# Performance work log

Hardware: AMD Instinct MI355X
Metric: run time of the kernel (lower is better)

## Reference

```python
import jax, jax.numpy as jnp
import numpy as np

B, L, D, K = 16, 4096, 256, 64
RHO, LAMBDA_Q, LAMBDA_S = 0.5, 1.0, 1.0


def setup_inputs() -> dict:
    key = jax.random.key(0)
    ks = jax.random.split(key, 16)
    s = 1.0 / np.sqrt(D)
    inp = {
        'q': jax.random.normal(ks[0], (B, D), jnp.float32),
        'r_pos': jax.random.normal(ks[1], (B, D), jnp.float32),
        'r_neg': jax.random.normal(ks[2], (B, D), jnp.float32),
        'h': jax.random.normal(ks[3], (B, L, D), jnp.float32),
        'rp': jax.random.normal(ks[4], (B, L, D), jnp.float32),
        'rn': jax.random.normal(ks[5], (B, L, D), jnp.float32),
        'lengths': jnp.maximum(1, jax.random.randint(ks[6], (B,), 0, L, jnp.int32)),
        'proto_idx': 3,
        'prototypes': jax.random.normal(ks[7], (K, D), jnp.float32),
        'W_hist_w': jax.random.normal(ks[8], (D, 2 * D), jnp.float32) * s,
        'W_hist_b': jnp.zeros((D,), jnp.float32),
        'Wq_w': jax.random.normal(ks[9], (D, D), jnp.float32) * s,
        'Wq_b': jnp.zeros((D,), jnp.float32),
        'Ws_w': jax.random.normal(ks[10], (D, D), jnp.float32) * s,
        'Ws_b': jnp.zeros((D,), jnp.float32),
    }
    return inp


def reference(q, r_pos, r_neg, h, rp, rn, lengths, proto_idx, prototypes,
              W_hist_w, W_hist_b, Wq_w, Wq_b, Ws_w, Ws_b):
    d = q.shape[-1]
    scale = 1.0 / jnp.sqrt(jnp.asarray(d, q.dtype))
    a = prototypes[proto_idx]                                   # [d]
    # gather + tanh-MLP over padded events: inp = [h, rp-rn] -> [B,L,2d]
    inp = jnp.concatenate([h, rp - rn], axis=-1)
    o = jnp.tanh(jnp.einsum('ble,de->bld', inp, W_hist_w) + W_hist_b)  # [B,L,d]
    # attention logits against prototype and query
    logits = (jnp.einsum('bld,d->bl', o, a)
              + RHO * jnp.einsum('bld,bd->bl', o, q)) * scale   # [B,L]
    mask = jnp.arange(o.shape[1])[None, :] < lengths[:, None]   # [B,L]
    logits = jnp.where(mask, logits, -1e30)
    alpha = jax.nn.softmax(logits, axis=1)
    s_q = jnp.einsum('bl,bld->bd', alpha, o)                    # [B,d]
    z = (a[None, :]
         + LAMBDA_Q * (q @ Wq_w.T + Wq_b)
         + LAMBDA_S * (s_q @ Ws_w.T + Ws_b))                    # [B,d]
    delta = jnp.sum(z * (r_pos - r_neg), axis=-1)               # [B]
    # BCE-with-logits against all-ones targets: mean softplus(-delta)
    l_pair = jnp.mean(jax.nn.softplus(-delta))
    return l_pair
```

## Files before the change

### kernel.cpp

```cpp
#include <hip/hip_runtime.h>

#define B_      16
#define L_      4096
#define D_      256
#define K2_     512
#define TILE_M  64
#define BK      64
#define KITERS  8
#define PSTRIDE 264

typedef float f32x4 __attribute__((ext_vector_type(4)));
typedef short bf16x8 __attribute__((ext_vector_type(8)));

__device__ __forceinline__ unsigned short f2bf(float x) {
    unsigned int u = __float_as_uint(x);
    u += 0x7FFF + ((u >> 16) & 1);
    return (unsigned short)(u >> 16);
}
__device__ __forceinline__ unsigned int pk2(float a, float b) {
    return (unsigned int)f2bf(a) | ((unsigned int)f2bf(b) << 16);
}
__device__ __forceinline__ bf16x8 pack8(f32x4 a, f32x4 b) {
    union { bf16x8 v; unsigned int u[4]; } r;
    r.u[0] = pk2(a[0], a[1]); r.u[1] = pk2(a[2], a[3]);
    r.u[2] = pk2(b[0], b[1]); r.u[3] = pk2(b[2], b[3]);
    return r.v;
}
__device__ __forceinline__ void gload_lds16(const void* g, void* l) {
    __builtin_amdgcn_global_load_lds(
        (const __attribute__((address_space(1))) unsigned int*)g,
        (__attribute__((address_space(3))) unsigned int*)l, 16, 0, 0);
}
__device__ __forceinline__ float fast_tanh(float x) {
    float e = __expf(2.0f * x);
    return 1.0f - __fdividef(2.0f, e + 1.0f);
}

__global__ __launch_bounds__(256) void prep_kernel(
    const float* __restrict__ Wh, const float* __restrict__ protos,
    const float* __restrict__ q, const int* __restrict__ pidx,
    const int* __restrict__ lengths,
    unsigned short* __restrict__ wsW, float* __restrict__ aeff,
    int* __restrict__ tiles, int* __restrict__ tileCnt)
{
    const int blk = blockIdx.x, tid = threadIdx.x;
    if (blk < 256) {
        int d  = blk;
        int e  = tid * 2;
        int t  = e >> 6;
        int kk = e & 63;
        float2 w = *reinterpret_cast<const float2*>(Wh + d * K2_ + e);
        unsigned int v = pk2(w.x, w.y);
        int dst = t * 32768 + ((d * 128 + kk * 2) ^ ((d & 7) << 4));
        *reinterpret_cast<unsigned int*>(reinterpret_cast<char*>(wsW) + dst) = v;
    } else if (blk < 272) {
        int b = blk - 256;
        int d = tid;
        int pi = pidx[0];
        aeff[b * D_ + d] = (protos[pi * D_ + d] + 0.5f * q[b * D_ + d]) * 0.0625f;
    } else {
        int nT = 0;
        if (tid < B_) nT = min(64, (lengths[tid] + TILE_M - 1) / TILE_M);
        int pre = 0, tot = 0;
#pragma unroll
        for (int j = 0; j < B_; ++j) {
            int v = __shfl(nT, j, 64);
            tot += v;
            if (j < tid) pre += v;
        }
        if (tid < B_) {
            for (int t = 0; t < nT; ++t) tiles[pre + t] = (tid << 16) | t;
        }
        if (tid == 0) tileCnt[0] = tot;
    }
}

__global__ __launch_bounds__(256, 2) void main_kernel(
    const float* __restrict__ h, const float* __restrict__ rp, const float* __restrict__ rn,
    const int* __restrict__ lengths, const unsigned short* __restrict__ wsW,
    const float* __restrict__ aeff, const float* __restrict__ bhist,
    float* __restrict__ partials, const int* __restrict__ tiles,
    const int* __restrict__ tileCnt)
{
    const int bid = blockIdx.x;
    if (bid >= tileCnt[0]) return;
    const int ent = tiles[bid];
    const int b   = ent >> 16;
    const int t   = ent & 0xFFFF;
    const int len = lengths[b];
    const int l0  = t * TILE_M;

    __shared__ __align__(16) char Bsm[65536];
    __shared__ float red[128];
    __shared__ float pbuf[64];
    __shared__ float solds[4 * 128];

    const int tid  = threadIdx.x;
    const int lane = tid & 63;
    const int wv   = tid >> 6;
    const int rg   = wv >> 1;
    const int ch   = wv & 1;
    const int r16  = lane & 15;
    const int kg   = lane >> 4;

    const size_t rowA0 = ((size_t)b * L_ + l0 + rg * 32 + r16) * D_ + kg * 8;

    const f32x4 zero4 = {0.f, 0.f, 0.f, 0.f};
    f32x4 acc[2][8];
#pragma unroll
    for (int m = 0; m < 2; ++m)
#pragma unroll
        for (int n = 0; n < 8; ++n) acc[m][n] = zero4;

    f32x4 pA[2][2][2], pB[2][2][2];
    bf16x8 frag[2][2];

    auto stageB = [&](int buf, int tk) {
        const char* bsrc = reinterpret_cast<const char*>(wsW) + tk * 32768;
        char* dst = Bsm + buf * 32768;
#pragma unroll
        for (int i = 0; i < 8; ++i) {
            int off = i * 4096 + wv * 1024;
            gload_lds16(bsrc + off + lane * 16, dst + off);
        }
    };
    auto loadA = [&](int tk) {
        if (tk < 4) {
            const float* p0 = h + rowA0 + tk * 64;
#pragma unroll
            for (int m = 0; m < 2; ++m) {
                const float* p = p0 + m * 16 * D_;
#pragma unroll
                for (int ks = 0; ks < 2; ++ks) {
                    pA[m][ks][0] = *reinterpret_cast<const f32x4*>(p + ks * 32);
                    pA[m][ks][1] = *reinterpret_cast<const f32x4*>(p + ks * 32 + 4);
                }
            }
        } else {
            size_t o0 = rowA0 + (tk - 4) * 64;
#pragma unroll
            for (int m = 0; m < 2; ++m) {
                size_t o = o0 + (size_t)m * 16 * D_;
#pragma unroll
                for (int ks = 0; ks < 2; ++ks) {
                    pA[m][ks][0] = *reinterpret_cast<const f32x4*>(rp + o + ks * 32);
                    pA[m][ks][1] = *reinterpret_cast<const f32x4*>(rp + o + ks * 32 + 4);
                    pB[m][ks][0] = *reinterpret_cast<const f32x4*>(rn + o + ks * 32);
                    pB[m][ks][1] = *reinterpret_cast<const f32x4*>(rn + o + ks * 32 + 4);
                }
            }
        }
    };
    auto cvtA = [&](int tk) {
#pragma unroll
        for (int m = 0; m < 2; ++m)
#pragma unroll
            for (int ks = 0; ks < 2; ++ks) {
                f32x4 v0, v1;
                if (tk < 4) { v0 = pA[m][ks][0]; v1 = pA[m][ks][1]; }
                else        { v0 = pA[m][ks][0] - pB[m][ks][0]; v1 = pA[m][ks][1] - pB[m][ks][1]; }
                frag[m][ks] = pack8(v0, v1);
            }
    };
    auto computeT = [&](int buf) {
        const char* Bb = Bsm + buf * 32768;
#pragma unroll
        for (int ks = 0; ks < 2; ++ks) {
#pragma unroll
            for (int nt = 0; nt < 8; ++nt) {
                int d   = ch * 128 + nt * 16 + r16;
                int off = (d * 128 + (ks * 32 + kg * 8) * 2) ^ ((d & 7) << 4);
                bf16x8 bfr = *reinterpret_cast<const bf16x8*>(Bb + off);
                acc[0][nt] = __builtin_amdgcn_mfma_f32_16x16x32_bf16(frag[0][ks], bfr, acc[0][nt], 0, 0, 0);
                acc[1][nt] = __builtin_amdgcn_mfma_f32_16x16x32_bf16(frag[1][ks], bfr, acc[1][nt], 0, 0, 0);
            }
        }
    };

    loadA(0);
    stageB(0, 0);
    cvtA(0);
    __syncthreads();

    int buf = 0;
    for (int tk = 0; tk < KITERS; ++tk) {
        const bool pf = (tk + 1) < KITERS;
        if (pf) { loadA(tk + 1); stageB(buf ^ 1, tk + 1); }
        __builtin_amdgcn_sched_barrier(0);
        computeT(buf);
        if (pf) cvtA(tk + 1);
        __syncthreads();
        buf ^= 1;
    }

    float av[8], bh[8];
#pragma unroll
    for (int nt = 0; nt < 8; ++nt) {
        int col = ch * 128 + nt * 16 + r16;
        av[nt] = aeff[b * D_ + col];
        bh[nt] = bhist[col];
    }
    float part[2][4];
#pragma unroll
    for (int m = 0; m < 2; ++m)
#pragma unroll
        for (int rgi = 0; rgi < 4; ++rgi) part[m][rgi] = 0.f;
#pragma unroll
    for (int m = 0; m < 2; ++m)
#pragma unroll
        for (int nt = 0; nt < 8; ++nt)
#pragma unroll
            for (int rgi = 0; rgi < 4; ++rgi) {
                float o = fast_tanh(acc[m][nt][rgi] + bh[nt]);
                acc[m][nt][rgi] = o;
                part[m][rgi] += o * av[nt];
            }
#pragma unroll
    for (int off = 1; off < 16; off <<= 1)
#pragma unroll
        for (int m = 0; m < 2; ++m)
#pragma unroll
            for (int rgi = 0; rgi < 4; ++rgi)
                part[m][rgi] += __shfl_xor(part[m][rgi], off, 64);
    if (r16 == 0) {
#pragma unroll
        for (int m = 0; m < 2; ++m)
#pragma unroll
            for (int rgi = 0; rgi < 4; ++rgi)
                red[ch * 64 + rg * 32 + m * 16 + kg * 4 + rgi] = part[m][rgi];
    }
    __syncthreads();

    float* pout = partials + (size_t)(b * 64 + t) * PSTRIDE;
    if (tid < 64) {
        int row = tid;
        float lg = red[row] + red[64 + row];
        bool valid = (l0 + row) < len;
        float mv = valid ? lg : -3.0e38f;
#pragma unroll
        for (int off = 1; off < 64; off <<= 1)
            mv = fmaxf(mv, __shfl_xor(mv, off, 64));
        float p = valid ? __expf(lg - mv) : 0.f;
        float sa = p;
#pragma unroll
        for (int off = 1; off < 64; off <<= 1)
            sa += __shfl_xor(sa, off, 64);
        pbuf[row] = p;
        if (tid == 0) { pout[0] = mv; pout[1] = sa; }
    }
    __syncthreads();

    float so[8];
#pragma unroll
    for (int nt = 0; nt < 8; ++nt) so[nt] = 0.f;
#pragma unroll
    for (int m = 0; m < 2; ++m)
#pragma unroll
        for (int rgi = 0; rgi < 4; ++rgi) {
            float p = pbuf[rg * 32 + m * 16 + kg * 4 + rgi];
#pragma unroll
            for (int nt = 0; nt < 8; ++nt)
                so[nt] += p * acc[m][nt][rgi];
        }
#pragma unroll
    for (int nt = 0; nt < 8; ++nt) {
        so[nt] += __shfl_xor(so[nt], 16, 64);
        so[nt] += __shfl_xor(so[nt], 32, 64);
    }
    if (lane < 16) {
#pragma unroll
        for (int nt = 0; nt < 8; ++nt)
            solds[wv * 128 + nt * 16 + lane] = so[nt];
    }
    __syncthreads();
    {
        int col = tid;
        int c2  = col >> 7, cl = col & 127;
        pout[2 + col] = solds[c2 * 128 + cl] + solds[(2 + c2) * 128 + cl];
    }
}

__global__ __launch_bounds__(256) void sq_kernel(
    const float* __restrict__ partials, const int* __restrict__ lengths,
    float* __restrict__ sqout)
{
    const int b   = blockIdx.x;
    const int tid = threadIdx.x;
    const int len = lengths[b];
    const int nT  = min(64, (len + TILE_M - 1) / TILE_M);

    __shared__ float mArr[64];
    __shared__ float sAArr[64];

    const float* pbase = partials + (size_t)b * 64 * PSTRIDE;
    if (tid < nT) {
        mArr[tid]  = pbase[(size_t)tid * PSTRIDE];
        sAArr[tid] = pbase[(size_t)tid * PSTRIDE + 1];
    }
    __syncthreads();

    float M = -3.0e38f;
    for (int t = 0; t < nT; ++t) M = fmaxf(M, mArr[t]);
    float den = 0.f, num = 0.f;
    for (int t = 0; t < nT; ++t) {
        float f = __expf(mArr[t] - M);
        den += f * sAArr[t];
        num += f * pbase[(size_t)t * PSTRIDE + 2 + tid];
    }
    sqout[b * D_ + tid] = num / den;
}

__global__ __launch_bounds__(256) void z_kernel(
    const float* __restrict__ q, const float* __restrict__ sq,
    const float* __restrict__ protos, const int* __restrict__ pidx,
    const float* __restrict__ Wq_w, const float* __restrict__ Wq_b,
    const float* __restrict__ Ws_w, const float* __restrict__ Ws_b,
    float* __restrict__ zout)
{
    const int r   = blockIdx.x;
    const int tid = threadIdx.x;
    const int bb  = tid >> 4;
    const int c   = tid & 15;
    const float4* wq = reinterpret_cast<const float4*>(Wq_w + (size_t)r * D_) + c * 4;
    const float4* ws = reinterpret_cast<const float4*>(Ws_w + (size_t)r * D_) + c * 4;
    const float4* qv = reinterpret_cast<const float4*>(q  + bb * D_) + c * 4;
    const float4* sv = reinterpret_cast<const float4*>(sq + bb * D_) + c * 4;
    float a = 0.f;
#pragma unroll
    for (int i = 0; i < 4; ++i) {
        float4 w1 = wq[i], w2 = ws[i], v1 = qv[i], v2 = sv[i];
        a += w1.x * v1.x + w1.y * v1.y + w1.z * v1.z + w1.w * v1.w;
        a += w2.x * v2.x + w2.y * v2.y + w2.z * v2.z + w2.w * v2.w;
    }
#pragma unroll
    for (int off = 1; off < 16; off <<= 1) a += __shfl_xor(a, off, 64);
    if (c == 0) {
        int pi = pidx[0];
        zout[bb * D_ + r] = protos[pi * D_ + r] + Wq_b[r] + Ws_b[r] + a;
    }
}

__global__ __launch_bounds__(256) void final_kernel(
    const float* __restrict__ zbuf,
    const float* __restrict__ rpos, const float* __restrict__ rneg,
    float* __restrict__ out)
{
    const int b   = blockIdx.x;
    const int tid = threadIdx.x;
    const int lane = tid & 63;
    const int wv   = tid >> 6;
    __shared__ float wsum[4];
    float v = zbuf[b * D_ + tid] * (rpos[b * D_ + tid] - rneg[b * D_ + tid]);
#pragma unroll
    for (int off = 1; off < 64; off <<= 1) v += __shfl_xor(v, off, 64);
    if (lane == 0) wsum[wv] = v;
    __syncthreads();
    if (tid == 0) {
        float delta = wsum[0] + wsum[1] + wsum[2] + wsum[3];
        float x = -delta;
        float sp = fmaxf(x, 0.f) + log1pf(__expf(-fabsf(x)));
        atomicAdd(out, sp * (1.0f / (float)B_));
    }
}

extern "C" void kernel_launch(void* const* d_in, const int* in_sizes, int n_in,
                              void* d_out, int out_size, void* d_ws, size_t ws_size,
                              hipStream_t stream) {
    const float* q       = (const float*)d_in[0];
    const float* r_pos   = (const float*)d_in[1];
    const float* r_neg   = (const float*)d_in[2];
    const float* h       = (const float*)d_in[3];
    const float* rp      = (const float*)d_in[4];
    const float* rn      = (const float*)d_in[5];
    const int*   lengths = (const int*)d_in[6];
    const int*   pidx    = (const int*)d_in[7];
    const float* protos  = (const float*)d_in[8];
    const float* Wh_w    = (const float*)d_in[9];
    const float* Wh_b    = (const float*)d_in[10];
    const float* Wq_w    = (const float*)d_in[11];
    const float* Wq_b    = (const float*)d_in[12];
    const float* Ws_w    = (const float*)d_in[13];
    const float* Ws_b    = (const float*)d_in[14];
    float* out = (float*)d_out;

    char* ws = (char*)d_ws;
    unsigned short* wsW = (unsigned short*)ws;
    float* aeff     = (float*)(ws + 262144);
    float* partials = (float*)(ws + 278528);
    int*   tiles    = (int*)(ws + 1359872);
    int*   tileCnt  = (int*)(ws + 1363968);
    float* sqws     = (float*)ws;
    float* zbuf     = (float*)(ws + 16384);

    hipMemsetAsync(out, 0, sizeof(float), stream);
    prep_kernel<<<dim3(273), dim3(256), 0, stream>>>(Wh_w, protos, q, pidx, lengths,
                                                     wsW, aeff, tiles, tileCnt);
    main_kernel<<<dim3(B_ * 64), dim3(256), 0, stream>>>(h, rp, rn, lengths, wsW, aeff, Wh_b,
                                                         partials, tiles, tileCnt);
    sq_kernel<<<dim3(B_), dim3(256), 0, stream>>>(partials, lengths, sqws);
    z_kernel<<<dim3(256), dim3(256), 0, stream>>>(q, sqws, protos, pidx,
                                                  Wq_w, Wq_b, Ws_w, Ws_b, zbuf);
    final_kernel<<<dim3(B_), dim3(256), 0, stream>>>(zbuf, r_pos, r_neg, out);
}
```

Before: 245.0 us.

## Use single-wave 32-row tiles reading weights directly from global memory

Replaces the 4-wave 64-row tile with LDS double-buffered weight staging by a single-wave block handling 32 rows and all 256 output columns. Weight fragments are read straight from global/L2 in a plain row-major bf16 layout, so there is no LDS and no block barriers. The softmax and weighted-sum epilogue is done entirely with wave shuffles. The sq reduction is split across 4 column blocks and 4 tile groups for more parallelism. The cost is twice as many blocks, heavier per-wave register use (32 accumulators), and repeated weight reads from cache with no pipelining of the A loads.

Result: slower. 291.3 us (+18.9%).

```diff
diff --git a/kernel.cpp b/kernel.cpp
--- a/kernel.cpp
+++ b/kernel.cpp
@@ -4,10 +4,10 @@
 #define L_      4096
 #define D_      256
 #define K2_     512
-#define TILE_M  64
-#define BK      64
+#define TILE_M  32
+#define MAXT    128
 #define KITERS  8
-#define PSTRIDE 264
+#define PSTRIDE 260
 
 typedef float f32x4 __attribute__((ext_vector_type(4)));
 typedef short bf16x8 __attribute__((ext_vector_type(8)));
@@ -26,11 +26,6 @@
     r.u[2] = pk2(b[0], b[1]); r.u[3] = pk2(b[2], b[3]);
     return r.v;
 }
-__device__ __forceinline__ void gload_lds16(const void* g, void* l) {
-    __builtin_amdgcn_global_load_lds(
-        (const __attribute__((address_space(1))) unsigned int*)g,
-        (__attribute__((address_space(3))) unsigned int*)l, 16, 0, 0);
-}
 __device__ __forceinline__ float fast_tanh(float x) {
     float e = __expf(2.0f * x);
     return 1.0f - __fdividef(2.0f, e + 1.0f);
@@ -40,19 +35,15 @@
     const float* __restrict__ Wh, const float* __restrict__ protos,
     const float* __restrict__ q, const int* __restrict__ pidx,
     const int* __restrict__ lengths,
-    unsigned short* __restrict__ wsW, float* __restrict__ aeff,
+    unsigned int* __restrict__ wsW32, float* __restrict__ aeff,
     int* __restrict__ tiles, int* __restrict__ tileCnt)
 {
     const int blk = blockIdx.x, tid = threadIdx.x;
     if (blk < 256) {
-        int d  = blk;
-        int e  = tid * 2;
-        int t  = e >> 6;
-        int kk = e & 63;
+        int d = blk;
+        int e = tid * 2;
         float2 w = *reinterpret_cast<const float2*>(Wh + d * K2_ + e);
-        unsigned int v = pk2(w.x, w.y);
-        int dst = t * 32768 + ((d * 128 + kk * 2) ^ ((d & 7) << 4));
-        *reinterpret_cast<unsigned int*>(reinterpret_cast<char*>(wsW) + dst) = v;
+        wsW32[d * 256 + tid] = pk2(w.x, w.y);
     } else if (blk < 272) {
         int b = blk - 256;
         int d = tid;
@@ -60,7 +51,7 @@
         aeff[b * D_ + d] = (protos[pi * D_ + d] + 0.5f * q[b * D_ + d]) * 0.0625f;
     } else {
         int nT = 0;
-        if (tid < B_) nT = min(64, (lengths[tid] + TILE_M - 1) / TILE_M);
+        if (tid < B_) nT = min(MAXT, (lengths[tid] + TILE_M - 1) / TILE_M);
         int pre = 0, tot = 0;
 #pragma unroll
         for (int j = 0; j < B_; ++j) {
@@ -75,7 +66,7 @@
     }
 }
 
-__global__ __launch_bounds__(256, 2) void main_kernel(
+__global__ __launch_bounds__(64, 2) void main_kernel(
     const float* __restrict__ h, const float* __restrict__ rp, const float* __restrict__ rn,
     const int* __restrict__ lengths, const unsigned short* __restrict__ wsW,
     const float* __restrict__ aeff, const float* __restrict__ bhist,
@@ -90,194 +81,128 @@
     const int len = lengths[b];
     const int l0  = t * TILE_M;
 
-    __shared__ __align__(16) char Bsm[65536];
-    __shared__ float red[128];
-    __shared__ float pbuf[64];
-    __shared__ float solds[4 * 128];
-
-    const int tid  = threadIdx.x;
-    const int lane = tid & 63;
-    const int wv   = tid >> 6;
-    const int rg   = wv >> 1;
-    const int ch   = wv & 1;
+    const int lane = threadIdx.x & 63;
     const int r16  = lane & 15;
     const int kg   = lane >> 4;
 
-    const size_t rowA0 = ((size_t)b * L_ + l0 + rg * 32 + r16) * D_ + kg * 8;
+    const size_t rowOff = ((size_t)(b * L_ + l0 + r16)) * D_ + kg * 8;
+    const float* hRow  = h  + rowOff;
+    const float* rpRow = rp + rowOff;
+    const float* rnRow = rn + rowOff;
+    const char* uB = reinterpret_cast<const char*>(wsW) + r16 * 1024 + kg * 16;
 
     const f32x4 zero4 = {0.f, 0.f, 0.f, 0.f};
-    f32x4 acc[2][8];
-#pragma unroll
-    for (int m = 0; m < 2; ++m)
-#pragma unroll
-        for (int n = 0; n < 8; ++n) acc[m][n] = zero4;
-
-    f32x4 pA[2][2][2], pB[2][2][2];
-    bf16x8 frag[2][2];
-
-    auto stageB = [&](int buf, int tk) {
-        const char* bsrc = reinterpret_cast<const char*>(wsW) + tk * 32768;
-        char* dst = Bsm + buf * 32768;
-#pragma unroll
-        for (int i = 0; i < 8; ++i) {
-            int off = i * 4096 + wv * 1024;
-            gload_lds16(bsrc + off + lane * 16, dst + off);
+    f32x4 acc0[16], acc1[16];
+#pragma unroll
+    for (int nt = 0; nt < 16; ++nt) { acc0[nt] = zero4; acc1[nt] = zero4; }
+
+#pragma unroll
+    for (int tk = 0; tk < 4; ++tk) {
+        bf16x8 frag[2][2];
+#pragma unroll
+        for (int mt = 0; mt < 2; ++mt)
+#pragma unroll
+            for (int ks = 0; ks < 2; ++ks) {
+                const float* p = hRow + mt * 16 * D_ + tk * 64 + ks * 32;
+                f32x4 v0 = *reinterpret_cast<const f32x4*>(p);
+                f32x4 v1 = *reinterpret_cast<const f32x4*>(p + 4);
+                frag[mt][ks] = pack8(v0, v1);
+            }
+#pragma unroll
+        for (int ks = 0; ks < 2; ++ks)
+#pragma unroll
+            for (int nt = 0; nt < 16; ++nt) {
+                bf16x8 bfr = *reinterpret_cast<const bf16x8*>(uB + nt * 16384 + tk * 128 + ks * 64);
+                acc0[nt] = __builtin_amdgcn_mfma_f32_16x16x32_bf16(frag[0][ks], bfr, acc0[nt], 0, 0, 0);
+                acc1[nt] = __builtin_amdgcn_mfma_f32_16x16x32_bf16(frag[1][ks], bfr, acc1[nt], 0, 0, 0);
+            }
+    }
+#pragma unroll
+    for (int tk = 4; tk < 8; ++tk) {
+        bf16x8 frag[2][2];
+#pragma unroll
+        for (int mt = 0; mt < 2; ++mt)
+#pragma unroll
+            for (int ks = 0; ks < 2; ++ks) {
+                const int off = mt * 16 * D_ + (tk - 4) * 64 + ks * 32;
+                f32x4 p0 = *reinterpret_cast<const f32x4*>(rpRow + off);
+                f32x4 p1 = *reinterpret_cast<const f32x4*>(rpRow + off + 4);
+                f32x4 n0 = *reinterpret_cast<const f32x4*>(rnRow + off);
+                f32x4 n1 = *reinterpret_cast<const f32x4*>(rnRow + off + 4);
+                frag[mt][ks] = pack8(p0 - n0, p1 - n1);
+            }
+#pragma unroll
+        for (int ks = 0; ks < 2; ++ks)
+#pragma unroll
+            for (int nt = 0; nt < 16; ++nt) {
+                bf16x8 bfr = *reinterpret_cast<const bf16x8*>(uB + nt * 16384 + tk * 128 + ks * 64);
+                acc0[nt] = __builtin_amdgcn_mfma_f32_16x16x32_bf16(frag[0][ks], bfr, acc0[nt], 0, 0, 0);
+                acc1[nt] = __builtin_amdgcn_mfma_f32_16x16x32_bf16(frag[1][ks], bfr, acc1[nt], 0, 0, 0);
+            }
+    }
+
+    float av[16], bhv[16];
+#pragma unroll
+    for (int nt = 0; nt < 16; ++nt) {
+        int col = nt * 16 + r16;
+        av[nt]  = aeff[b * D_ + col];
+        bhv[nt] = bhist[col];
+    }
+    float part0[4] = {0.f, 0.f, 0.f, 0.f};
+    float part1[4] = {0.f, 0.f, 0.f, 0.f};
+#pragma unroll
+    for (int nt = 0; nt < 16; ++nt)
+#pragma unroll
+        for (int rgi = 0; rgi < 4; ++rgi) {
+            float o0 = fast_tanh(acc0[nt][rgi] + bhv[nt]);
+            float o1 = fast_tanh(acc1[nt][rgi] + bhv[nt]);
+            acc0[nt][rgi] = o0;
+            acc1[nt][rgi] = o1;
+            part0[rgi] += o0 * av[nt];
+            part1[rgi] += o1 * av[nt];
         }
-    };
-    auto loadA = [&](int tk) {
-        if (tk < 4) {
-            const float* p0 = h + rowA0 + tk * 64;
-#pragma unroll
-            for (int m = 0; m < 2; ++m) {
-                const float* p = p0 + m * 16 * D_;
-#pragma unroll
-                for (int ks = 0; ks < 2; ++ks) {
-                    pA[m][ks][0] = *reinterpret_cast<const f32x4*>(p + ks * 32);
-                    pA[m][ks][1] = *reinterpret_cast<const f32x4*>(p + ks * 32 + 4);
-                }
-            }
-        } else {
-            size_t o0 = rowA0 + (tk - 4) * 64;
-#pragma unroll
-            for (int m = 0; m < 2; ++m) {
-                size_t o = o0 + (size_t)m * 16 * D_;
-#pragma unroll
-                for (int ks = 0; ks < 2; ++ks) {
-                    pA[m][ks][0] = *reinterpret_cast<const f32x4*>(rp + o + ks * 32);
-                    pA[m][ks][1] = *reinterpret_cast<const f32x4*>(rp + o + ks * 32 + 4);
-                    pB[m][ks][0] = *reinterpret_cast<const f32x4*>(rn + o + ks * 32);
-                    pB[m][ks][1] = *reinterpret_cast<const f32x4*>(rn + o + ks * 32 + 4);
-                }
-            }
+#pragma unroll
+    for (int off = 1; off < 16; off <<= 1)
+#pragma unroll
+        for (int rgi = 0; rgi < 4; ++rgi) {
+            part0[rgi] += __shfl_xor(part0[rgi], off, 64);
+            part1[rgi] += __shfl_xor(part1[rgi], off, 64);
         }
-    };
-    auto cvtA = [&](int tk) {
-#pragma unroll
-        for (int m = 0; m < 2; ++m)
-#pragma unroll
-            for (int ks = 0; ks < 2; ++ks) {
-                f32x4 v0, v1;
-                if (tk < 4) { v0 = pA[m][ks][0]; v1 = pA[m][ks][1]; }
-                else        { v0 = pA[m][ks][0] - pB[m][ks][0]; v1 = pA[m][ks][1] - pB[m][ks][1]; }
-                frag[m][ks] = pack8(v0, v1);
-            }
-    };
-    auto computeT = [&](int buf) {
-        const char* Bb = Bsm + buf * 32768;
-#pragma unroll
-        for (int ks = 0; ks < 2; ++ks) {
-#pragma unroll
-            for (int nt = 0; nt < 8; ++nt) {
-                int d   = ch * 128 + nt * 16 + r16;
-                int off = (d * 128 + (ks * 32 + kg * 8) * 2) ^ ((d & 7) << 4);
-                bf16x8 bfr = *reinterpret_cast<const bf16x8*>(Bb + off);
-                acc[0][nt] = __builtin_amdgcn_mfma_f32_16x16x32_bf16(frag[0][ks], bfr, acc[0][nt], 0, 0, 0);
-                acc[1][nt] = __builtin_amdgcn_mfma_f32_16x16x32_bf16(frag[1][ks], bfr, acc[1][nt], 0, 0, 0);
-            }
-        }
-    };
-
-    loadA(0);
-    stageB(0, 0);
-    cvtA(0);
-    __syncthreads();
-
-    int buf = 0;
-    for (int tk = 0; tk < KITERS; ++tk) {
-        const bool pf = (tk + 1) < KITERS;
-        if (pf) { loadA(tk + 1); stageB(buf ^ 1, tk + 1); }
-        __builtin_amdgcn_sched_barrier(0);
-        computeT(buf);
-        if (pf) cvtA(tk + 1);
-        __syncthreads();
-        buf ^= 1;
-    }
-
-    float av[8], bh[8];
-#pragma unroll
-    for (int nt = 0; nt < 8; ++nt) {
-        int col = ch * 128 + nt * 16 + r16;
-        av[nt] = aeff[b * D_ + col];
-        bh[nt] = bhist[col];
-    }
-    float part[2][4];
-#pragma unroll
-    for (int m = 0; m < 2; ++m)
-#pragma unroll
-        for (int rgi = 0; rgi < 4; ++rgi) part[m][rgi] = 0.f;
-#pragma unroll
-    for (int m = 0; m < 2; ++m)
-#pragma unroll
-        for (int nt = 0; nt < 8; ++nt)
-#pragma unroll
-            for (int rgi = 0; rgi < 4; ++rgi) {
-                float o = fast_tanh(acc[m][nt][rgi] + bh[nt]);
-                acc[m][nt][rgi] = o;
-                part[m][rgi] += o * av[nt];
-            }
-#pragma unroll
-    for (int off = 1; off < 16; off <<= 1)
-#pragma unroll
-        for (int m = 0; m < 2; ++m)
-#pragma unroll
-            for (int rgi = 0; rgi < 4; ++rgi)
-                part[m][rgi] += __shfl_xor(part[m][rgi], off, 64);
-    if (r16 == 0) {
-#pragma unroll
-        for (int m = 0; m < 2; ++m)
-#pragma unroll
-            for (int rgi = 0; rgi < 4; ++rgi)
-                red[ch * 64 + rg * 32 + m * 16 + kg * 4 + rgi] = part[m][rgi];
-    }
-    __syncthreads();
-
-    float* pout = partials + (size_t)(b * 64 + t) * PSTRIDE;
-    if (tid < 64) {
-        int row = tid;
-        float lg = red[row] + red[64 + row];
-        bool valid = (l0 + row) < len;
-        float mv = valid ? lg : -3.0e38f;
-#pragma unroll
-        for (int off = 1; off < 64; off <<= 1)
-            mv = fmaxf(mv, __shfl_xor(mv, off, 64));
-        float p = valid ? __expf(lg - mv) : 0.f;
-        float sa = p;
-#pragma unroll
-        for (int off = 1; off < 64; off <<= 1)
-            sa += __shfl_xor(sa, off, 64);
-        pbuf[row] = p;
-        if (tid == 0) { pout[0] = mv; pout[1] = sa; }
-    }
-    __syncthreads();
-
-    float so[8];
-#pragma unroll
-    for (int nt = 0; nt < 8; ++nt) so[nt] = 0.f;
-#pragma unroll
-    for (int m = 0; m < 2; ++m)
-#pragma unroll
-        for (int rgi = 0; rgi < 4; ++rgi) {
-            float p = pbuf[rg * 32 + m * 16 + kg * 4 + rgi];
-#pragma unroll
-            for (int nt = 0; nt < 8; ++nt)
-                so[nt] += p * acc[m][nt][rgi];
-        }
-#pragma unroll
-    for (int nt = 0; nt < 8; ++nt) {
-        so[nt] += __shfl_xor(so[nt], 16, 64);
-        so[nt] += __shfl_xor(so[nt], 32, 64);
-    }
-    if (lane < 16) {
-#pragma unroll
-        for (int nt = 0; nt < 8; ++nt)
-            solds[wv * 128 + nt * 16 + lane] = so[nt];
-    }
-    __syncthreads();
-    {
-        int col = tid;
-        int c2  = col >> 7, cl = col & 127;
-        pout[2 + col] = solds[c2 * 128 + cl] + solds[(2 + c2) * 128 + cl];
-    }
+    float mv = -3.0e38f;
+    bool val0[4], val1[4];
+#pragma unroll
+    for (int rgi = 0; rgi < 4; ++rgi) {
+        int row = kg * 4 + rgi;
+        val0[rgi] = (l0 + row) < len;
+        val1[rgi] = (l0 + 16 + row) < len;
+        if (val0[rgi]) mv = fmaxf(mv, part0[rgi]);
+        if (val1[rgi]) mv = fmaxf(mv, part1[rgi]);
+    }
+    mv = fmaxf(mv, __shfl_xor(mv, 16, 64));
+    mv = fmaxf(mv, __shfl_xor(mv, 32, 64));
+    float p0[4], p1[4];
+    float sa = 0.f;
+#pragma unroll
+    for (int rgi = 0; rgi < 4; ++rgi) {
+        p0[rgi] = val0[rgi] ? __expf(part0[rgi] - mv) : 0.f;
+        p1[rgi] = val1[rgi] ? __expf(part1[rgi] - mv) : 0.f;
+        sa += p0[rgi] + p1[rgi];
+    }
+    sa += __shfl_xor(sa, 16, 64);
+    sa += __shfl_xor(sa, 32, 64);
+
+    float* pout = partials + (size_t)(b * MAXT + t) * PSTRIDE;
+#pragma unroll
+    for (int nt = 0; nt < 16; ++nt) {
+        float so = 0.f;
+#pragma unroll
+        for (int rgi = 0; rgi < 4; ++rgi)
+            so += p0[rgi] * acc0[nt][rgi] + p1[rgi] * acc1[nt][rgi];
+        so += __shfl_xor(so, 16, 64);
+        so += __shfl_xor(so, 32, 64);
+        if (kg == 0) pout[2 + nt * 16 + r16] = so;
+    }
+    if (lane == 0) { pout[0] = mv; pout[1] = sa; }
 }
 
 __global__ __launch_bounds__(256) void sq_kernel(
@@ -285,14 +210,18 @@
     float* __restrict__ sqout)
 {
     const int b   = blockIdx.x;
+    const int cy  = blockIdx.y;
     const int tid = threadIdx.x;
+    const int c   = tid & 63;
+    const int tg  = tid >> 6;
     const int len = lengths[b];
-    const int nT  = min(64, (len + TILE_M - 1) / TILE_M);
-
-    __shared__ float mArr[64];
-    __shared__ float sAArr[64];
-
-    const float* pbase = partials + (size_t)b * 64 * PSTRIDE;
+    const int nT  = min(MAXT, (len + TILE_M - 1) / TILE_M);
+
+    __shared__ float mArr[MAXT];
+    __shared__ float sAArr[MAXT];
+    __shared__ float psum[4][64];
+
+    const float* pbase = partials + (size_t)b * MAXT * PSTRIDE;
     if (tid < nT) {
         mArr[tid]  = pbase[(size_t)tid * PSTRIDE];
         sAArr[tid] = pbase[(size_t)tid * PSTRIDE + 1];
@@ -301,13 +230,17 @@
 
     float M = -3.0e38f;
     for (int t = 0; t < nT; ++t) M = fmaxf(M, mArr[t]);
-    float den = 0.f, num = 0.f;
-    for (int t = 0; t < nT; ++t) {
-        float f = __expf(mArr[t] - M);
-        den += f * sAArr[t];
-        num += f * pbase[(size_t)t * PSTRIDE + 2 + tid];
-    }
-    sqout[b * D_ + tid] = num / den;
+    float den = 0.f;
+    for (int t = 0; t < nT; ++t) den += __expf(mArr[t] - M) * sAArr[t];
+
+    float num = 0.f;
+    for (int t = tg; t < nT; t += 4)
+        num += __expf(mArr[t] - M) * pbase[(size_t)t * PSTRIDE + 2 + cy * 64 + c];
+    psum[tg][c] = num;
+    __syncthreads();
+    if (tg == 0)
+        sqout[b * D_ + cy * 64 + c] =
+            (psum[0][c] + psum[1][c] + psum[2][c] + psum[3][c]) / den;
 }
 
 __global__ __launch_bounds__(256) void z_kernel(
@@ -387,17 +320,17 @@
     unsigned short* wsW = (unsigned short*)ws;
     float* aeff     = (float*)(ws + 262144);
     float* partials = (float*)(ws + 278528);
-    int*   tiles    = (int*)(ws + 1359872);
-    int*   tileCnt  = (int*)(ws + 1363968);
+    int*   tiles    = (int*)(ws + 2408448);
+    int*   tileCnt  = (int*)(ws + 2416640);
     float* sqws     = (float*)ws;
     float* zbuf     = (float*)(ws + 16384);
 
     hipMemsetAsync(out, 0, sizeof(float), stream);
     prep_kernel<<<dim3(273), dim3(256), 0, stream>>>(Wh_w, protos, q, pidx, lengths,
-                                                     wsW, aeff, tiles, tileCnt);
-    main_kernel<<<dim3(B_ * 64), dim3(256), 0, stream>>>(h, rp, rn, lengths, wsW, aeff, Wh_b,
-                                                         partials, tiles, tileCnt);
-    sq_kernel<<<dim3(B_), dim3(256), 0, stream>>>(partials, lengths, sqws);
+                                                     (unsigned int*)wsW, aeff, tiles, tileCnt);
+    main_kernel<<<dim3(B_ * MAXT), dim3(64), 0, stream>>>(h, rp, rn, lengths, wsW, aeff, Wh_b,
+                                                          partials, tiles, tileCnt);
+    sq_kernel<<<dim3(B_, 4), dim3(256), 0, stream>>>(partials, lengths, sqws);
     z_kernel<<<dim3(256), dim3(256), 0, stream>>>(q, sqws, protos, pidx,
                                                   Wq_w, Wq_b, Ws_w, Ws_b, zbuf);
     final_kernel<<<dim3(B_), dim3(256), 0, stream>>>(zbuf, r_pos, r_neg, out);
```
